# Performance work log

Measured on AMD Instinct MI355X. Metric: run time of the kernel, lower is better.

## Reference

```python
import jax, jax.numpy as jnp
import numpy as np

N_E, N_C, N_DL, N_IT, N_EP, N_HA, N_CA, N_AS = 11964, 188, 100, 7, 100, 10, 10, 7
D = 128
B, S = 256, 400
N_V = N_E + 1      # hypergraph vertices (exercises)
N_HE = N_C + 1     # hyperedges (concepts)
MEMB = 3           # concept memberships per exercise
BN_EPS = 1e-5


def _hg_v2v_mean(X, pair_v, pair_e):
    # HGNN+ smoothing: vertex -> hyperedge (mean) -> vertex (mean)
    ones_e = jnp.ones(pair_e.shape, X.dtype)
    e_deg = jnp.clip(jax.ops.segment_sum(ones_e, pair_e, num_segments=N_HE), 1.0)
    v_deg = jnp.clip(jax.ops.segment_sum(ones_e, pair_v, num_segments=N_V), 1.0)
    E = jax.ops.segment_sum(X[pair_v], pair_e, num_segments=N_HE) / e_deg[:, None]
    return jax.ops.segment_sum(E[pair_e], pair_v, num_segments=N_V) / v_deg[:, None]


def _hgnnp_conv(X, W, b, gamma, beta, mean, var, pair_v, pair_e, is_last):
    X = X @ W + b
    X = (X - mean) * jax.lax.rsqrt(var + BN_EPS) * gamma + beta  # eval-mode BN
    X = _hg_v2v_mean(X, pair_v, pair_e)
    if not is_last:
        X = jax.nn.relu(X)
    return X


def setup_inputs() -> dict:
    key = jax.random.key(0)
    ks = jax.random.split(key, 32)
    inp = {}
    inp['input_e'] = jax.random.randint(ks[0], (B, S), 0, N_V)
    inp['input_ed'] = jax.random.randint(ks[1], (B, S), 0, N_DL + 1)
    inp['input_ep'] = jax.random.randint(ks[2], (B, S), 0, N_EP + 1)
    inp['input_a'] = jax.random.randint(ks[3], (B, S), 0, 2)
    inp['input_as'] = jax.random.randint(ks[4], (B, S), 0, N_AS + 1)
    inp['input_ha'] = jax.random.randint(ks[5], (B, S), 0, N_HA + 1)
    inp['input_ca'] = jax.random.randint(ks[6], (B, S), 0, N_CA + 1)
    inp['input_it'] = jax.random.randint(ks[7], (B, S), 0, N_IT + 1)
    inp['deliver_h'] = jnp.zeros((B, D), jnp.float32)
    # hypergraph incidence (exercise-concept Q-matrix edges)
    rng = np.random.default_rng(0)
    inp['pair_v'] = jnp.asarray(np.repeat(np.arange(N_V), MEMB))
    inp['pair_e'] = jnp.asarray(rng.integers(0, N_HE, size=N_V * MEMB))
    inp['ec_map'] = jax.random.randint(ks[8], (N_V,), 0, N_HE)
    inp['ecd_map'] = jax.random.randint(ks[9], (N_V,), 0, N_DL + 1)
    # embedding tables (xavier-ish scale)
    def emb(k, n):
        return jax.random.normal(k, (n, D), jnp.float32) * 0.05
    inp['e_table'] = emb(ks[10], N_V)
    inp['c_table'] = emb(ks[11], N_HE)
    inp['ed_table'] = emb(ks[12], N_DL + 1)
    inp['cd_table'] = emb(ks[13], N_DL + 1)
    inp['a_table'] = emb(ks[14], 2)
    inp['it_table'] = emb(ks[15], N_IT + 1)
    inp['ep_table'] = emb(ks[16], N_EP + 1)
    inp['ha_table'] = emb(ks[17], N_HA + 1)
    inp['ca_table'] = emb(ks[18], N_CA + 1)
    inp['as_table'] = emb(ks[19], N_AS + 1)
    # HGNNP conv 1 & 2
    def lin(k, din, dout):
        return jax.random.normal(k, (din, dout), jnp.float32) * (1.0 / np.sqrt(din))
    inp['W1'] = lin(ks[20], D, D); inp['b1'] = jnp.zeros((D,), jnp.float32)
    inp['g1'] = jnp.ones((D,), jnp.float32); inp['be1'] = jnp.zeros((D,), jnp.float32)
    inp['m1'] = jnp.zeros((D,), jnp.float32); inp['v1'] = jnp.ones((D,), jnp.float32)
    inp['W2'] = lin(ks[21], D, D); inp['b2'] = jnp.zeros((D,), jnp.float32)
    inp['g2'] = jnp.ones((D,), jnp.float32); inp['be2'] = jnp.zeros((D,), jnp.float32)
    inp['m2'] = jnp.zeros((D,), jnp.float32); inp['v2'] = jnp.ones((D,), jnp.float32)
    # linear_i: (d_e + d_dl + d_ep + d_c + d_dl) -> d_x
    inp['Wi'] = lin(ks[22], 5 * D, D); inp['bi'] = jnp.zeros((D,), jnp.float32)
    # GRU knowledge-state cell: input = concat(x, a_emb) -> 2D, hidden D, 3 gates
    inp['Wg'] = lin(ks[23], 2 * D, 3 * D)
    inp['Ug'] = lin(ks[24], D, 3 * D)
    inp['bg'] = jnp.zeros((3 * D,), jnp.float32)
    # linear_predicting_e: d_x -> 1
    inp['We'] = lin(ks[25], D, 1); inp['beo'] = jnp.zeros((1,), jnp.float32)
    # linear_predicting_s: 4*d -> 1
    inp['Ws'] = lin(ks[26], 4 * D, 1); inp['bs'] = jnp.zeros((1,), jnp.float32)
    return inp


def reference(input_e, input_ed, input_ep, input_a, input_as, input_ha, input_ca, input_it,
              deliver_h, pair_v, pair_e, ec_map, ecd_map,
              e_table, c_table, ed_table, cd_table, a_table, it_table, ep_table,
              ha_table, ca_table, as_table,
              W1, b1, g1, be1, m1, v1, W2, b2, g2, be2, m2, v2,
              Wi, bi, Wg, Ug, bg, We, beo, Ws, bs):
    # 2-layer HGNN+ over the exercise hypergraph
    X = _hgnnp_conv(e_table, W1, b1, g1, be1, m1, v1, pair_v, pair_e, is_last=False)
    X = _hgnnp_conv(X, W2, b2, g2, be2, m2, v2, pair_v, pair_e, is_last=True)
    # embedding gathers  [B,S,D]
    e_emb = X[input_e]
    c_emb = c_table[ec_map[input_e]]
    cd_emb = cd_table[ecd_map[input_e]]
    ed_emb = ed_table[input_ed]
    ep_emb = ep_table[input_ep]
    x = jnp.tanh(jnp.concatenate([e_emb, ed_emb, ep_emb, c_emb, cd_emb], -1) @ Wi + bi)  # [B,S,D]
    a_emb = a_table[input_a]
    xs = jnp.moveaxis(jnp.concatenate([x, a_emb], -1), 1, 0)  # [S,B,2D]
    xp = jnp.moveaxis(x, 1, 0)                                # [S,B,D]

    def step(h, inputs):
        xin, xq = inputs
        y = jax.nn.sigmoid((h * xq) @ We + beo)[..., 0]  # predict from prior knowledge state
        gi = xin @ Wg + bg
        gh = h @ Ug
        iz, ir, inn = jnp.split(gi, 3, -1)
        hz, hr, hn = jnp.split(gh, 3, -1)
        z = jax.nn.sigmoid(iz + hz)
        r = jax.nn.sigmoid(ir + hr)
        n = jnp.tanh(inn + r * hn)
        return (1.0 - z) * n + z * h, y

    _, ys = jax.lax.scan(step, deliver_h, (xs, xp))
    pred_main = jnp.moveaxis(ys, 0, 1)  # [B,S]
    s_in = jnp.concatenate([ha_table[input_ha], ca_table[input_ca],
                            as_table[input_as], it_table[input_it]], -1)
    pred_s = jax.nn.sigmoid(s_in @ Ws + bs)[..., 0]  # [B,S]
    return pred_s, pred_main
```

## Files before the change

kernel.cpp:

```cpp
#include <hip/hip_runtime.h>

#define N_V   11965
#define N_HE  189
#define NPAIR 35895
#define BB    256
#define SS    400
#define DD    128
#define BSR   102400

typedef __bf16 bf16x8 __attribute__((ext_vector_type(8)));
typedef float  f32x4  __attribute__((ext_vector_type(4)));

__device__ __forceinline__ ushort f2bf(float f) {
    unsigned x = __float_as_uint(f);
    return (ushort)((x + 0x7FFFu + ((x >> 16) & 1u)) >> 16);
}
__device__ __forceinline__ float bf2f(ushort u) { return __uint_as_float(((unsigned)u) << 16); }
__device__ __forceinline__ float sigm(float x) { return 1.f / (1.f + __expf(-x)); }
__device__ __forceinline__ float tanh_f(float x) { return 2.f * sigm(2.f * x) - 1.f; }
__device__ __forceinline__ float blo(unsigned u) { return __uint_as_float(u << 16); }
__device__ __forceinline__ float bhi(unsigned u) { return __uint_as_float(u); }

struct P1Args {
    const int* pair_e;
    const float *b1, *g1, *be1, *m1, *v1;
    const float *b2, *g2, *be2, *m2, *v2;
    const float *W1, *W2, *Wi, *Wg, *Ug;
    const float *ed_t, *ep_t, *c_t, *cd_t, *a_t, *bi, *bg;
    const float *ha_t, *ca_t, *as_t, *it_t, *Ws;
    int* e_deg;
    float* aff;
    ushort *W1T, *W2T, *WiTe, *WgT, *UgT;
    float *edW, *epW, *cW, *cdW, *agi, *sd;
};

__global__ __launch_bounds__(384) void p1_kernel(P1Args A) {
    int bid = blockIdx.x, t = threadIdx.x;
    if (bid == 0) {
        if (t < 128) {
            float s = A.g1[t] * rsqrtf(A.v1[t] + 1e-5f);
            A.aff[t] = s;
            A.aff[128 + t] = A.b1[t] * s + A.be1[t] - A.m1[t] * s;
        } else if (t < 256) {
            int d = t - 128;
            float s = A.g2[d] * rsqrtf(A.v2[d] + 1e-5f);
            A.aff[256 + d] = s;
            A.aff[384 + d] = A.b2[d] * s + A.be2[d] - A.m2[d] * s;
        }
        return;
    }
    bid -= 1;
    if (bid < 94) {
        int p = bid * 384 + t;
        if (p < NPAIR) atomicAdd(&A.e_deg[A.pair_e[p]], 1);
        return;
    }
    bid -= 94;
    if (bid < 43) {
        int i = bid * 384 + t;
        if (i < 16384) { int k = i >> 7, n = i & 127; A.W1T[n * 128 + k] = f2bf(A.W1[i]); }
        return;
    }
    bid -= 43;
    if (bid < 43) {
        int i = bid * 384 + t;
        if (i < 16384) { int k = i >> 7, n = i & 127; A.W2T[n * 128 + k] = f2bf(A.W2[i]); }
        return;
    }
    bid -= 43;
    if (bid < 43) {
        int i = bid * 384 + t;
        if (i < 16384) { int k = i >> 7, n = i & 127; A.WiTe[n * 128 + k] = f2bf(A.Wi[i]); }
        return;
    }
    bid -= 43;
    if (bid < 128) {
        int i = bid * 384 + t;
        if (i < 49152) { int k = i / 384, n = i % 384; A.WgT[n * 128 + k] = f2bf(A.Wg[i]); }
        return;
    }
    bid -= 128;
    if (bid < 128) {
        int i = bid * 384 + t;
        if (i < 49152) { int k = i / 384, n = i % 384; A.UgT[n * 128 + k] = f2bf(A.Ug[i]); }
        return;
    }
    bid -= 128;
    if (bid < 101) {
        if (t < 128) {
            float acc = 0.f;
            for (int k = 0; k < 128; ++k)
                acc += A.ed_t[bid * 128 + k] * A.Wi[(128 + k) * 128 + t];
            A.edW[bid * 128 + t] = acc + A.bi[t];
        }
        return;
    }
    bid -= 101;
    if (bid < 101) {
        if (t < 128) {
            float acc = 0.f;
            for (int k = 0; k < 128; ++k)
                acc += A.ep_t[bid * 128 + k] * A.Wi[(256 + k) * 128 + t];
            A.epW[bid * 128 + t] = acc;
        }
        return;
    }
    bid -= 101;
    if (bid < 189) {
        if (t < 128) {
            float acc = 0.f;
            for (int k = 0; k < 128; ++k)
                acc += A.c_t[bid * 128 + k] * A.Wi[(384 + k) * 128 + t];
            A.cW[bid * 128 + t] = acc;
        }
        return;
    }
    bid -= 189;
    if (bid < 101) {
        if (t < 128) {
            float acc = 0.f;
            for (int k = 0; k < 128; ++k)
                acc += A.cd_t[bid * 128 + k] * A.Wi[(512 + k) * 128 + t];
            A.cdW[bid * 128 + t] = acc;
        }
        return;
    }
    bid -= 101;
    if (bid < 2) {
        float acc = 0.f;
        for (int k = 0; k < 128; ++k)
            acc += A.a_t[bid * 128 + k] * A.Wg[(128 + k) * 384 + t];
        A.agi[bid * 384 + t] = acc + A.bg[t];
        return;
    }
    bid -= 2;
    {
        int r = bid;
        const float* tab; int woff, row;
        if (r < 11)      { tab = A.ha_t; row = r;      woff = 0;   }
        else if (r < 22) { tab = A.ca_t; row = r - 11; woff = 128; }
        else if (r < 30) { tab = A.as_t; row = r - 22; woff = 256; }
        else             { tab = A.it_t; row = r - 30; woff = 384; }
        if (t < 64) {
            float p = tab[row * 128 + t] * A.Ws[woff + t]
                    + tab[row * 128 + 64 + t] * A.Ws[woff + 64 + t];
            #pragma unroll
            for (int o = 32; o > 0; o >>= 1) p += __shfl_xor(p, o);
            if (t == 0) A.sd[r] = p;
        }
    }
}

__global__ void cvt_kernel(const float* __restrict__ src, ushort* __restrict__ dst, int n) {
    int i = blockIdx.x * 256 + threadIdx.x;
    if (i < n) dst[i] = f2bf(src[i]);
}

__global__ void csr_prefix(const int* __restrict__ e_deg, int* __restrict__ start) {
    __shared__ int sc[256];
    int t = threadIdx.x;
    int d = (t < N_HE) ? e_deg[t] : 0;
    sc[t] = d;
    __syncthreads();
    for (int off = 1; off < 256; off <<= 1) {
        int v = (t >= off) ? sc[t - off] : 0;
        __syncthreads();
        sc[t] += v;
        __syncthreads();
    }
    if (t < N_HE) start[t] = sc[t] - d;
    if (t == N_HE - 1) start[N_HE] = sc[t];
}

__global__ void csr_fill(const int* __restrict__ pair_e, const int* __restrict__ pair_v,
                         const int* __restrict__ start, int* __restrict__ cursor,
                         int* __restrict__ list) {
    int p = blockIdx.x * 384 + threadIdx.x;
    if (p >= NPAIR) return;
    int e = pair_e[p];
    int pos = atomicAdd(&cursor[e], 1);
    list[start[e] + pos] = pair_v[p];
}

template <int NT>
__global__ __launch_bounds__(256) void gemm_mfma(
    const ushort* __restrict__ Amat, const ushort* __restrict__ BT,
    float* __restrict__ out, int M,
    const float* __restrict__ colS, const float* __restrict__ colB,
    const float* __restrict__ agi, const int* __restrict__ aidx) {
    const int N = NT * 16;
    int lane = threadIdx.x & 63, wave = threadIdx.x >> 6;
    int q = lane >> 4, c = lane & 15;
    int rowbase = blockIdx.x * 64 + wave * 16;
    int arow = rowbase + c;
    if (arow > M - 1) arow = M - 1;
    f32x4 acc[NT];
#pragma unroll
    for (int i = 0; i < NT; ++i) acc[i] = (f32x4){0.f, 0.f, 0.f, 0.f};
#pragma unroll
    for (int ko = 0; ko < 4; ++ko) {
        bf16x8 af = *(const bf16x8*)(Amat + (size_t)arow * 128 + ko * 32 + q * 8);
#pragma unroll
        for (int nt = 0; nt < NT; ++nt) {
            bf16x8 bfr = *(const bf16x8*)(BT + (size_t)(nt * 16 + c) * 128 + ko * 32 + q * 8);
            acc[nt] = __builtin_amdgcn_mfma_f32_16x16x32_bf16(af, bfr, acc[nt], 0, 0, 0);
        }
    }
#pragma unroll
    for (int nt = 0; nt < NT; ++nt) {
        int col = nt * 16 + c;
        float s = colS ? colS[col] : 1.f;
        float bb = colB ? colB[col] : 0.f;
#pragma unroll
        for (int r = 0; r < 4; ++r) {
            int row = rowbase + q * 4 + r;
            if (row < M) {
                float v = acc[nt][r] * s + bb;
                if (agi) v += agi[aidx[row] * N + col];
                out[(size_t)row * N + col] = v;
            }
        }
    }
}

__global__ __launch_bounds__(512) void edge_mean(const float* __restrict__ Y,
                                                 const int* __restrict__ list,
                                                 const int* __restrict__ start,
                                                 float* __restrict__ E) {
    __shared__ float red[4][128];
    int e = blockIdx.x;
    int d = threadIdx.x & 127, g = threadIdx.x >> 7;
    int s0 = start[e], n = start[e + 1] - s0;
    float acc = 0.f;
    for (int i = g; i < n; i += 4) acc += Y[(size_t)list[s0 + i] * DD + d];
    red[g][d] = acc;
    __syncthreads();
    if (g == 0) {
        float v = red[0][d] + red[1][d] + red[2][d] + red[3][d];
        E[e * DD + d] = v / (float)(n > 0 ? n : 1);
    }
}

__global__ void v_mean(const float* __restrict__ E, const int* __restrict__ pair_e,
                       ushort* __restrict__ Xo, int relu) {
    int idx = blockIdx.x * 256 + threadIdx.x;
    if (idx >= N_V * DD) return;
    int v = idx >> 7, d = idx & 127;
    float a = E[pair_e[3 * v] * DD + d] + E[pair_e[3 * v + 1] * DD + d] +
              E[pair_e[3 * v + 2] * DD + d];
    a *= (1.f / 3.f);
    if (relu) a = fmaxf(a, 0.f);
    Xo[idx] = f2bf(a);
}

__global__ void k3_kernel(const int* __restrict__ in_e, const int* __restrict__ in_ed,
                          const int* __restrict__ in_ep, const float* __restrict__ XW,
                          const float* __restrict__ cW, const float* __restrict__ cdW,
                          const float* __restrict__ edW, const float* __restrict__ epW,
                          const int* __restrict__ ec_map, const int* __restrict__ ecd_map,
                          ushort* __restrict__ xbf) {
    int idx = blockIdx.x * 256 + threadIdx.x;
    if (idx >= BSR * DD) return;
    int row = idx >> 7, d = idx & 127;
    int e = in_e[row];
    float v = XW[(size_t)e * DD + d] + cW[ec_map[e] * DD + d] + cdW[ecd_map[e] * DD + d] +
              edW[in_ed[row] * DD + d] + epW[in_ep[row] * DD + d];
    xbf[idx] = f2bf(tanh_f(v));
}

__global__ void pred_s_kernel(const int* __restrict__ ha, const int* __restrict__ ca,
                              const int* __restrict__ as_, const int* __restrict__ it,
                              const float* __restrict__ sd, const float* __restrict__ bs,
                              float* __restrict__ out) {
    int i = blockIdx.x * 256 + threadIdx.x;
    if (i >= BSR) return;
    float v = sd[ha[i]] + sd[11 + ca[i]] + sd[22 + as_[i]] + sd[30 + it[i]] + bs[0];
    out[i] = sigm(v);
}

__global__ void
__attribute__((amdgpu_flat_work_group_size(768, 768)))
gru_scan(
    const float* __restrict__ gi, const ushort* __restrict__ xb,
    const ushort* __restrict__ UgT, const float* __restrict__ h0,
    const float* __restrict__ We, const float* __restrict__ beo_p,
    float* __restrict__ out) {
    __shared__ __align__(16) float h_s[128];
    __shared__ float p_s[128];
    __shared__ float pp[4][392];
    int b = blockIdx.x, t = threadIdx.x;
    int kq = t / 192;
    int cp = t % 192;
    const uint4* WA = (const uint4*)(UgT + (size_t)cp * 128 + kq * 32);
    const uint4* WB = (const uint4*)(UgT + (size_t)(cp + 192) * 128 + kq * 32);
    uint4 A0 = WA[0], A1 = WA[1], A2 = WA[2], A3 = WA[3];
    uint4 B0 = WB[0], B1 = WB[1], B2 = WB[2], B3 = WB[3];
    unsigned a0 = A0.x, a1 = A0.y, a2 = A0.z, a3 = A0.w;
    unsigned a4 = A1.x, a5 = A1.y, a6 = A1.z, a7 = A1.w;
    unsigned a8 = A2.x, a9 = A2.y, a10 = A2.z, a11 = A2.w;
    unsigned a12 = A3.x, a13 = A3.y, a14 = A3.z, a15 = A3.w;
    unsigned c0 = B0.x, c1 = B0.y, c2 = B0.z, c3 = B0.w;
    unsigned c4 = B1.x, c5 = B1.y, c6 = B1.z, c7 = B1.w;
    unsigned c8 = B2.x, c9 = B2.y, c10 = B2.z, c11 = B2.w;
    unsigned c12 = B3.x, c13 = B3.y, c14 = B3.z, c15 = B3.w;
    float beo = beo_p[0];
    float wev = 0.f, hreg = 0.f;
    if (t < 128) {
        wev = We[t];
        hreg = h0[b * 128 + t];
        h_s[t] = hreg;
    }
    const float* gip = gi + (size_t)b * SS * 384;
    const ushort* xp = xb + (size_t)b * SS * 128;
    float gz_nx = 0.f, gr_nx = 0.f, gn_nx = 0.f, xw_nx = 0.f;
    if (t < 128) {
        gz_nx = gip[t];
        gr_nx = gip[128 + t];
        gn_nx = gip[256 + t];
        xw_nx = bf2f(xp[t]) * wev;
    }
    float* omain = out + BSR + b * SS;
    __syncthreads();
    for (int s = 0; s < SS; ++s) {
#define PINA(X) asm volatile("" : "+a"(X));
        PINA(a0) PINA(a1) PINA(a2) PINA(a3) PINA(a4) PINA(a5) PINA(a6) PINA(a7)
        PINA(a8) PINA(a9) PINA(a10) PINA(a11) PINA(a12) PINA(a13) PINA(a14) PINA(a15)
        PINA(c0) PINA(c1) PINA(c2) PINA(c3) PINA(c4) PINA(c5) PINA(c6) PINA(c7)
        PINA(c8) PINA(c9) PINA(c10) PINA(c11) PINA(c12) PINA(c13) PINA(c14) PINA(c15)
#undef PINA
        float gz = gz_nx, gr = gr_nx, gn = gn_nx, xw = xw_nx;
        if (s + 1 < SS && t < 128) {
            const float* g2 = gip + (size_t)(s + 1) * 384;
            gz_nx = g2[t];
            gr_nx = g2[128 + t];
            gn_nx = g2[256 + t];
            xw_nx = bf2f(xp[(size_t)(s + 1) * 128 + t]) * wev;
        }
        const float4* h4 = (const float4*)h_s + kq * 8;
        float accA = 0.f, accB = 0.f;
#define FB2(HI, U0, U1, U2, U3, V0, V1, V2, V3) { \
        float4 hv0 = h4[HI], hv1 = h4[HI + 1]; \
        accA = fmaf(hv0.x, blo(U0), accA); accA = fmaf(hv0.y, bhi(U0), accA); \
        accA = fmaf(hv0.z, blo(U1), accA); accA = fmaf(hv0.w, bhi(U1), accA); \
        accA = fmaf(hv1.x, blo(U2), accA); accA = fmaf(hv1.y, bhi(U2), accA); \
        accA = fmaf(hv1.z, blo(U3), accA); accA = fmaf(hv1.w, bhi(U3), accA); \
        accB = fmaf(hv0.x, blo(V0), accB); accB = fmaf(hv0.y, bhi(V0), accB); \
        accB = fmaf(hv0.z, blo(V1), accB); accB = fmaf(hv0.w, bhi(V1), accB); \
        accB = fmaf(hv1.x, blo(V2), accB); accB = fmaf(hv1.y, bhi(V2), accB); \
        accB = fmaf(hv1.z, blo(V3), accB); accB = fmaf(hv1.w, bhi(V3), accB); }
        FB2(0, a0, a1, a2, a3, c0, c1, c2, c3)
        FB2(2, a4, a5, a6, a7, c4, c5, c6, c7)
        FB2(4, a8, a9, a10, a11, c8, c9, c10, c11)
        FB2(6, a12, a13, a14, a15, c12, c13, c14, c15)
#undef FB2
        pp[kq][cp] = accA;
        pp[kq][cp + 192] = accB;
        if (t >= 704 && s > 0) {
            int l = t - 704;
            float pv = p_s[l] + p_s[l + 64];
#pragma unroll
            for (int o = 32; o > 0; o >>= 1) pv += __shfl_xor(pv, o);
            if (l == 0) omain[s - 1] = sigm(pv + beo);
        }
        __syncthreads();
        if (t < 128) {
            float Sz = pp[0][t] + pp[1][t] + pp[2][t] + pp[3][t];
            float Sr = pp[0][128 + t] + pp[1][128 + t] + pp[2][128 + t] + pp[3][128 + t];
            float Sn = pp[0][256 + t] + pp[1][256 + t] + pp[2][256 + t] + pp[3][256 + t];
            float z = sigm(gz + Sz);
            float r = sigm(gr + Sr);
            float n = tanh_f(gn + r * Sn);
            p_s[t] = hreg * xw;
            hreg = (1.f - z) * n + z * hreg;
            h_s[t] = hreg;
        }
        __syncthreads();
    }
    if (t >= 704) {
        int l = t - 704;
        float pv = p_s[l] + p_s[l + 64];
#pragma unroll
        for (int o = 32; o > 0; o >>= 1) pv += __shfl_xor(pv, o);
        if (l == 0) omain[SS - 1] = sigm(pv + beo);
    }
}

extern "C" void kernel_launch(void* const* d_in, const int* in_sizes, int n_in,
                              void* d_out, int out_size, void* d_ws, size_t ws_size,
                              hipStream_t stream) {
    const int* in_e   = (const int*)d_in[0];
    const int* in_ed  = (const int*)d_in[1];
    const int* in_ep  = (const int*)d_in[2];
    const int* in_a   = (const int*)d_in[3];
    const int* in_as  = (const int*)d_in[4];
    const int* in_ha  = (const int*)d_in[5];
    const int* in_ca  = (const int*)d_in[6];
    const int* in_it  = (const int*)d_in[7];
    const float* deliver_h = (const float*)d_in[8];
    const int* pair_v = (const int*)d_in[9];
    const int* pair_e = (const int*)d_in[10];
    const int* ec_map = (const int*)d_in[11];
    const int* ecd_map= (const int*)d_in[12];
    const float* e_table  = (const float*)d_in[13];
    const float* c_table  = (const float*)d_in[14];
    const float* ed_table = (const float*)d_in[15];
    const float* cd_table = (const float*)d_in[16];
    const float* a_table  = (const float*)d_in[17];
    const float* it_table = (const float*)d_in[18];
    const float* ep_table = (const float*)d_in[19];
    const float* ha_table = (const float*)d_in[20];
    const float* ca_table = (const float*)d_in[21];
    const float* as_table = (const float*)d_in[22];
    const float* W1 = (const float*)d_in[23];
    const float* b1 = (const float*)d_in[24];
    const float* g1 = (const float*)d_in[25];
    const float* be1= (const float*)d_in[26];
    const float* m1 = (const float*)d_in[27];
    const float* v1 = (const float*)d_in[28];
    const float* W2 = (const float*)d_in[29];
    const float* b2 = (const float*)d_in[30];
    const float* g2 = (const float*)d_in[31];
    const float* be2= (const float*)d_in[32];
    const float* m2 = (const float*)d_in[33];
    const float* v2 = (const float*)d_in[34];
    const float* Wi = (const float*)d_in[35];
    const float* bi = (const float*)d_in[36];
    const float* Wg = (const float*)d_in[37];
    const float* Ug = (const float*)d_in[38];
    const float* bg = (const float*)d_in[39];
    const float* We = (const float*)d_in[40];
    const float* beo= (const float*)d_in[41];
    const float* Ws = (const float*)d_in[42];
    const float* bs = (const float*)d_in[43];
    float* out = (float*)d_out;
    char* ws = (char*)d_ws;

    size_t off = 0;
    auto alloc = [&](size_t bytes) { size_t o = off; off += (bytes + 255) & ~(size_t)255; return o; };
    size_t o_degcur = alloc(378 * 4);
    size_t o_start  = alloc(190 * 4);
    size_t o_list   = alloc((size_t)NPAIR * 4);
    size_t o_aff    = alloc(512 * 4);
    size_t o_W1T    = alloc(16384 * 2);
    size_t o_W2T    = alloc(16384 * 2);
    size_t o_WiTe   = alloc(16384 * 2);
    size_t o_WgT    = alloc(49152 * 2);
    size_t o_UgT    = alloc(49152 * 2);
    size_t o_edW    = alloc(101 * 128 * 4);
    size_t o_epW    = alloc(101 * 128 * 4);
    size_t o_cW     = alloc(189 * 128 * 4);
    size_t o_cdW    = alloc(101 * 128 * 4);
    size_t o_agi    = alloc(2 * 384 * 4);
    size_t o_sd     = alloc(38 * 4);
    size_t o_etb    = alloc((size_t)N_V * DD * 2);
    size_t o_E      = alloc((size_t)N_HE * DD * 4);
    size_t o_Y      = alloc((size_t)N_V * DD * 4);
    size_t o_X1     = alloc((size_t)N_V * DD * 2);
    size_t o_X2     = alloc((size_t)N_V * DD * 2);
    size_t o_XW     = alloc((size_t)N_V * DD * 4);
    size_t o_xbf    = alloc((size_t)BSR * DD * 2);
    size_t o_gi     = alloc((size_t)BSR * 384 * 4);

    int*    e_deg  = (int*)(ws + o_degcur);
    int*    cursor = e_deg + 189;
    int*    startp = (int*)(ws + o_start);
    int*    listp  = (int*)(ws + o_list);
    float*  aff    = (float*)(ws + o_aff);
    ushort* W1T    = (ushort*)(ws + o_W1T);
    ushort* W2T    = (ushort*)(ws + o_W2T);
    ushort* WiTe   = (ushort*)(ws + o_WiTe);
    ushort* WgT    = (ushort*)(ws + o_WgT);
    ushort* UgTp   = (ushort*)(ws + o_UgT);
    float*  edW    = (float*)(ws + o_edW);
    float*  epW    = (float*)(ws + o_epW);
    float*  cW     = (float*)(ws + o_cW);
    float*  cdW    = (float*)(ws + o_cdW);
    float*  agi    = (float*)(ws + o_agi);
    float*  sd     = (float*)(ws + o_sd);
    ushort* e_tb   = (ushort*)(ws + o_etb);
    float*  E      = (float*)(ws + o_E);
    float*  Y      = (float*)(ws + o_Y);
    ushort* X1b    = (ushort*)(ws + o_X1);
    ushort* X2b    = (ushort*)(ws + o_X2);
    float*  XW     = (float*)(ws + o_XW);
    ushort* xbf    = (ushort*)(ws + o_xbf);
    float*  gi     = (float*)(ws + o_gi);

    hipMemsetAsync(ws + o_degcur, 0, 378 * 4, stream);

    P1Args pa;
    pa.pair_e = pair_e;
    pa.b1 = b1; pa.g1 = g1; pa.be1 = be1; pa.m1 = m1; pa.v1 = v1;
    pa.b2 = b2; pa.g2 = g2; pa.be2 = be2; pa.m2 = m2; pa.v2 = v2;
    pa.W1 = W1; pa.W2 = W2; pa.Wi = Wi; pa.Wg = Wg; pa.Ug = Ug;
    pa.ed_t = ed_table; pa.ep_t = ep_table; pa.c_t = c_table; pa.cd_t = cd_table;
    pa.a_t = a_table; pa.bi = bi; pa.bg = bg;
    pa.ha_t = ha_table; pa.ca_t = ca_table; pa.as_t = as_table; pa.it_t = it_table; pa.Ws = Ws;
    pa.e_deg = e_deg; pa.aff = aff;
    pa.W1T = W1T; pa.W2T = W2T; pa.WiTe = WiTe; pa.WgT = WgT; pa.UgT = UgTp;
    pa.edW = edW; pa.epW = epW; pa.cW = cW; pa.cdW = cdW; pa.agi = agi; pa.sd = sd;
    p1_kernel<<<1012, 384, 0, stream>>>(pa);

    cvt_kernel<<<(N_V * DD + 255) / 256, 256, 0, stream>>>(e_table, e_tb, N_V * DD);
    csr_prefix<<<1, 256, 0, stream>>>(e_deg, startp);
    csr_fill<<<94, 384, 0, stream>>>(pair_e, pair_v, startp, cursor, listp);

    pred_s_kernel<<<(BSR + 255) / 256, 256, 0, stream>>>(in_ha, in_ca, in_as, in_it, sd, bs, out);

    gemm_mfma<8><<<(N_V + 63) / 64, 256, 0, stream>>>(e_tb, W1T, Y, N_V, aff, aff + 128,
                                                      nullptr, nullptr);
    edge_mean<<<N_HE, 512, 0, stream>>>(Y, listp, startp, E);
    v_mean<<<(N_V * DD + 255) / 256, 256, 0, stream>>>(E, pair_e, X1b, 1);
    gemm_mfma<8><<<(N_V + 63) / 64, 256, 0, stream>>>(X1b, W2T, Y, N_V, aff + 256, aff + 384,
                                                      nullptr, nullptr);
    edge_mean<<<N_HE, 512, 0, stream>>>(Y, listp, startp, E);
    v_mean<<<(N_V * DD + 255) / 256, 256, 0, stream>>>(E, pair_e, X2b, 0);
    gemm_mfma<8><<<(N_V + 63) / 64, 256, 0, stream>>>(X2b, WiTe, XW, N_V, nullptr, nullptr,
                                                      nullptr, nullptr);
    k3_kernel<<<(BSR * DD + 255) / 256, 256, 0, stream>>>(in_e, in_ed, in_ep, XW, cW, cdW, edW,
                                                          epW, ec_map, ecd_map, xbf);
    gemm_mfma<24><<<BSR / 64, 256, 0, stream>>>(xbf, WgT, gi, BSR, nullptr, nullptr, agi, in_a);
    gru_scan<<<BB, 768, 0, stream>>>(gi, xbf, UgTp, deliver_h, We, beo, out);
}
```

Measured before the change: 976.5 us.

## Fuse setup kernels, store GRU input gates in bf16, vectorize gather kernel

Folds the e_table bf16 conversion into the setup kernel, merges the CSR prefix and fill into one kernel, and moves the pred_s computation into the gate GEMM epilogue, cutting the number of launches. The precomputed GRU input-gate tensor (BSR×384) is now written and read as bf16 instead of fp32, halving that large memory round trip. The embedding gather and tanh kernel now processes four columns per thread with float4 loads. Storing the gates in bf16 adds rounding error to the recurrent inputs.

```diff
diff --git a/kernel.cpp b/kernel.cpp
--- a/kernel.cpp
+++ b/kernel.cpp
@@ -7,6 +7,7 @@
 #define SS    400
 #define DD    128
 #define BSR   102400
+#define NVD   (N_V * DD)
 
 typedef __bf16 bf16x8 __attribute__((ext_vector_type(8)));
 typedef float  f32x4  __attribute__((ext_vector_type(4)));
@@ -25,12 +26,12 @@
     const int* pair_e;
     const float *b1, *g1, *be1, *m1, *v1;
     const float *b2, *g2, *be2, *m2, *v2;
-    const float *W1, *W2, *Wi, *Wg, *Ug;
+    const float *W1, *W2, *Wi, *Wg, *Ug, *e_t;
     const float *ed_t, *ep_t, *c_t, *cd_t, *a_t, *bi, *bg;
     const float *ha_t, *ca_t, *as_t, *it_t, *Ws;
     int* e_deg;
     float* aff;
-    ushort *W1T, *W2T, *WiTe, *WgT, *UgT;
+    ushort *W1T, *W2T, *WiTe, *WgT, *UgT, *e_tb;
     float *edW, *epW, *cW, *cdW, *agi, *sd;
 };
 
@@ -86,6 +87,17 @@
         return;
     }
     bid -= 128;
+    if (bid < 998) {
+        int i4 = bid * 1536 + t * 4;
+        if (i4 < NVD) {
+            float4 v = *(const float4*)(A.e_t + i4);
+            ushort4 o;
+            o.x = f2bf(v.x); o.y = f2bf(v.y); o.z = f2bf(v.z); o.w = f2bf(v.w);
+            *(ushort4*)(A.e_tb + i4) = o;
+        }
+        return;
+    }
+    bid -= 998;
     if (bid < 101) {
         if (t < 128) {
             float acc = 0.f;
@@ -151,75 +163,108 @@
     }
 }
 
-__global__ void cvt_kernel(const float* __restrict__ src, ushort* __restrict__ dst, int n) {
-    int i = blockIdx.x * 256 + threadIdx.x;
-    if (i < n) dst[i] = f2bf(src[i]);
-}
-
-__global__ void csr_prefix(const int* __restrict__ e_deg, int* __restrict__ start) {
+__global__ __launch_bounds__(384) void csr_build(
+    const int* __restrict__ e_deg, const int* __restrict__ pair_e,
+    const int* __restrict__ pair_v, int* __restrict__ start,
+    int* __restrict__ cursor, int* __restrict__ list) {
     __shared__ int sc[256];
+    __shared__ int sx[256];
     int t = threadIdx.x;
-    int d = (t < N_HE) ? e_deg[t] : 0;
-    sc[t] = d;
+    int d = 0;
+    if (t < 256) { d = (t < N_HE) ? e_deg[t] : 0; sc[t] = d; }
     __syncthreads();
     for (int off = 1; off < 256; off <<= 1) {
-        int v = (t >= off) ? sc[t - off] : 0;
+        int v = (t < 256 && t >= off) ? sc[t - off] : 0;
         __syncthreads();
-        sc[t] += v;
+        if (t < 256) sc[t] += v;
         __syncthreads();
     }
-    if (t < N_HE) start[t] = sc[t] - d;
-    if (t == N_HE - 1) start[N_HE] = sc[t];
-}
-
-__global__ void csr_fill(const int* __restrict__ pair_e, const int* __restrict__ pair_v,
-                         const int* __restrict__ start, int* __restrict__ cursor,
-                         int* __restrict__ list) {
-    int p = blockIdx.x * 384 + threadIdx.x;
-    if (p >= NPAIR) return;
-    int e = pair_e[p];
-    int pos = atomicAdd(&cursor[e], 1);
-    list[start[e] + pos] = pair_v[p];
-}
-
-template <int NT>
-__global__ __launch_bounds__(256) void gemm_mfma(
+    if (t < 256) sx[t] = sc[t] - d;
+    __syncthreads();
+    if (blockIdx.x == 0) {
+        if (t < N_HE) start[t] = sx[t];
+        if (t == 0) start[N_HE] = sc[N_HE - 1];
+    }
+    int p = blockIdx.x * 384 + t;
+    if (p < NPAIR) {
+        int e = pair_e[p];
+        int pos = atomicAdd(&cursor[e], 1);
+        list[sx[e] + pos] = pair_v[p];
+    }
+}
+
+__global__ __launch_bounds__(256) void gemm_mfma8(
     const ushort* __restrict__ Amat, const ushort* __restrict__ BT,
     float* __restrict__ out, int M,
-    const float* __restrict__ colS, const float* __restrict__ colB,
-    const float* __restrict__ agi, const int* __restrict__ aidx) {
-    const int N = NT * 16;
+    const float* __restrict__ colS, const float* __restrict__ colB) {
     int lane = threadIdx.x & 63, wave = threadIdx.x >> 6;
     int q = lane >> 4, c = lane & 15;
     int rowbase = blockIdx.x * 64 + wave * 16;
     int arow = rowbase + c;
     if (arow > M - 1) arow = M - 1;
-    f32x4 acc[NT];
-#pragma unroll
-    for (int i = 0; i < NT; ++i) acc[i] = (f32x4){0.f, 0.f, 0.f, 0.f};
+    f32x4 acc[8];
+#pragma unroll
+    for (int i = 0; i < 8; ++i) acc[i] = (f32x4){0.f, 0.f, 0.f, 0.f};
 #pragma unroll
     for (int ko = 0; ko < 4; ++ko) {
         bf16x8 af = *(const bf16x8*)(Amat + (size_t)arow * 128 + ko * 32 + q * 8);
 #pragma unroll
-        for (int nt = 0; nt < NT; ++nt) {
+        for (int nt = 0; nt < 8; ++nt) {
             bf16x8 bfr = *(const bf16x8*)(BT + (size_t)(nt * 16 + c) * 128 + ko * 32 + q * 8);
             acc[nt] = __builtin_amdgcn_mfma_f32_16x16x32_bf16(af, bfr, acc[nt], 0, 0, 0);
         }
     }
 #pragma unroll
-    for (int nt = 0; nt < NT; ++nt) {
+    for (int nt = 0; nt < 8; ++nt) {
         int col = nt * 16 + c;
         float s = colS ? colS[col] : 1.f;
         float bb = colB ? colB[col] : 0.f;
 #pragma unroll
         for (int r = 0; r < 4; ++r) {
             int row = rowbase + q * 4 + r;
-            if (row < M) {
-                float v = acc[nt][r] * s + bb;
-                if (agi) v += agi[aidx[row] * N + col];
-                out[(size_t)row * N + col] = v;
-            }
-        }
+            if (row < M) out[(size_t)row * 128 + col] = acc[nt][r] * s + bb;
+        }
+    }
+}
+
+__global__ __launch_bounds__(256) void gemm_gi(
+    const ushort* __restrict__ Amat, const ushort* __restrict__ BT,
+    ushort* __restrict__ out, const float* __restrict__ agi,
+    const int* __restrict__ aidx,
+    const int* __restrict__ ha, const int* __restrict__ ca,
+    const int* __restrict__ as_, const int* __restrict__ it,
+    const float* __restrict__ sd, const float* __restrict__ bs,
+    float* __restrict__ outs) {
+    int lane = threadIdx.x & 63, wave = threadIdx.x >> 6;
+    int q = lane >> 4, c = lane & 15;
+    int rowbase = blockIdx.x * 64 + wave * 16;
+    int arow = rowbase + c;
+    f32x4 acc[24];
+#pragma unroll
+    for (int i = 0; i < 24; ++i) acc[i] = (f32x4){0.f, 0.f, 0.f, 0.f};
+#pragma unroll
+    for (int ko = 0; ko < 4; ++ko) {
+        bf16x8 af = *(const bf16x8*)(Amat + (size_t)arow * 128 + ko * 32 + q * 8);
+#pragma unroll
+        for (int nt = 0; nt < 24; ++nt) {
+            bf16x8 bfr = *(const bf16x8*)(BT + (size_t)(nt * 16 + c) * 128 + ko * 32 + q * 8);
+            acc[nt] = __builtin_amdgcn_mfma_f32_16x16x32_bf16(af, bfr, acc[nt], 0, 0, 0);
+        }
+    }
+#pragma unroll
+    for (int nt = 0; nt < 24; ++nt) {
+        int col = nt * 16 + c;
+#pragma unroll
+        for (int r = 0; r < 4; ++r) {
+            int row = rowbase + q * 4 + r;
+            float v = acc[nt][r] + agi[aidx[row] * 384 + col];
+            out[(size_t)row * 384 + col] = f2bf(v);
+        }
+    }
+    if (threadIdx.x < 64) {
+        int row = blockIdx.x * 64 + threadIdx.x;
+        float v = sd[ha[row]] + sd[11 + ca[row]] + sd[22 + as_[row]] + sd[30 + it[row]] + bs[0];
+        outs[row] = sigm(v);
     }
 }
 
@@ -244,7 +289,7 @@
 __global__ void v_mean(const float* __restrict__ E, const int* __restrict__ pair_e,
                        ushort* __restrict__ Xo, int relu) {
     int idx = blockIdx.x * 256 + threadIdx.x;
-    if (idx >= N_V * DD) return;
+    if (idx >= NVD) return;
     int v = idx >> 7, d = idx & 127;
     float a = E[pair_e[3 * v] * DD + d] + E[pair_e[3 * v + 1] * DD + d] +
               E[pair_e[3 * v + 2] * DD + d];
@@ -260,28 +305,26 @@
                           const int* __restrict__ ec_map, const int* __restrict__ ecd_map,
                           ushort* __restrict__ xbf) {
     int idx = blockIdx.x * 256 + threadIdx.x;
-    if (idx >= BSR * DD) return;
-    int row = idx >> 7, d = idx & 127;
+    if (idx >= BSR * 32) return;
+    int row = idx >> 5, dq = (idx & 31) << 2;
     int e = in_e[row];
-    float v = XW[(size_t)e * DD + d] + cW[ec_map[e] * DD + d] + cdW[ecd_map[e] * DD + d] +
-              edW[in_ed[row] * DD + d] + epW[in_ep[row] * DD + d];
-    xbf[idx] = f2bf(tanh_f(v));
-}
-
-__global__ void pred_s_kernel(const int* __restrict__ ha, const int* __restrict__ ca,
-                              const int* __restrict__ as_, const int* __restrict__ it,
-                              const float* __restrict__ sd, const float* __restrict__ bs,
-                              float* __restrict__ out) {
-    int i = blockIdx.x * 256 + threadIdx.x;
-    if (i >= BSR) return;
-    float v = sd[ha[i]] + sd[11 + ca[i]] + sd[22 + as_[i]] + sd[30 + it[i]] + bs[0];
-    out[i] = sigm(v);
+    float4 a = *(const float4*)(XW + (size_t)e * DD + dq);
+    float4 b = *(const float4*)(cW + ec_map[e] * DD + dq);
+    float4 c = *(const float4*)(cdW + ecd_map[e] * DD + dq);
+    float4 d = *(const float4*)(edW + in_ed[row] * DD + dq);
+    float4 g = *(const float4*)(epW + in_ep[row] * DD + dq);
+    ushort4 o;
+    o.x = f2bf(tanh_f(a.x + b.x + c.x + d.x + g.x));
+    o.y = f2bf(tanh_f(a.y + b.y + c.y + d.y + g.y));
+    o.z = f2bf(tanh_f(a.z + b.z + c.z + d.z + g.z));
+    o.w = f2bf(tanh_f(a.w + b.w + c.w + d.w + g.w));
+    *(ushort4*)(xbf + (size_t)row * DD + dq) = o;
 }
 
 __global__ void
 __attribute__((amdgpu_flat_work_group_size(768, 768)))
 gru_scan(
-    const float* __restrict__ gi, const ushort* __restrict__ xb,
+    const ushort* __restrict__ gi, const ushort* __restrict__ xb,
     const ushort* __restrict__ UgT, const float* __restrict__ h0,
     const float* __restrict__ We, const float* __restrict__ beo_p,
     float* __restrict__ out) {
@@ -310,13 +353,13 @@
         hreg = h0[b * 128 + t];
         h_s[t] = hreg;
     }
-    const float* gip = gi + (size_t)b * SS * 384;
+    const ushort* gip = gi + (size_t)b * SS * 384;
     const ushort* xp = xb + (size_t)b * SS * 128;
     float gz_nx = 0.f, gr_nx = 0.f, gn_nx = 0.f, xw_nx = 0.f;
     if (t < 128) {
-        gz_nx = gip[t];
-        gr_nx = gip[128 + t];
-        gn_nx = gip[256 + t];
+        gz_nx = bf2f(gip[t]);
+        gr_nx = bf2f(gip[128 + t]);
+        gn_nx = bf2f(gip[256 + t]);
         xw_nx = bf2f(xp[t]) * wev;
     }
     float* omain = out + BSR + b * SS;
@@ -330,10 +373,10 @@
 #undef PINA
         float gz = gz_nx, gr = gr_nx, gn = gn_nx, xw = xw_nx;
         if (s + 1 < SS && t < 128) {
-            const float* g2 = gip + (size_t)(s + 1) * 384;
-            gz_nx = g2[t];
-            gr_nx = g2[128 + t];
-            gn_nx = g2[256 + t];
+            const ushort* g2 = gip + (size_t)(s + 1) * 384;
+            gz_nx = bf2f(g2[t]);
+            gr_nx = bf2f(g2[128 + t]);
+            gn_nx = bf2f(g2[256 + t]);
             xw_nx = bf2f(xp[(size_t)(s + 1) * 128 + t]) * wev;
         }
         const float4* h4 = (const float4*)h_s + kq * 8;
@@ -452,14 +495,14 @@
     size_t o_cdW    = alloc(101 * 128 * 4);
     size_t o_agi    = alloc(2 * 384 * 4);
     size_t o_sd     = alloc(38 * 4);
-    size_t o_etb    = alloc((size_t)N_V * DD * 2);
+    size_t o_etb    = alloc((size_t)NVD * 2);
     size_t o_E      = alloc((size_t)N_HE * DD * 4);
-    size_t o_Y      = alloc((size_t)N_V * DD * 4);
-    size_t o_X1     = alloc((size_t)N_V * DD * 2);
-    size_t o_X2     = alloc((size_t)N_V * DD * 2);
-    size_t o_XW     = alloc((size_t)N_V * DD * 4);
+    size_t o_Y      = alloc((size_t)NVD * 4);
+    size_t o_X1     = alloc((size_t)NVD * 2);
+    size_t o_X2     = alloc((size_t)NVD * 2);
+    size_t o_XW     = alloc((size_t)NVD * 4);
     size_t o_xbf    = alloc((size_t)BSR * DD * 2);
-    size_t o_gi     = alloc((size_t)BSR * 384 * 4);
+    size_t o_gi     = alloc((size_t)BSR * 384 * 2);
 
     int*    e_deg  = (int*)(ws + o_degcur);
     int*    cursor = e_deg + 189;
@@ -484,7 +527,7 @@
     ushort* X2b    = (ushort*)(ws + o_X2);
     float*  XW     = (float*)(ws + o_XW);
     ushort* xbf    = (ushort*)(ws + o_xbf);
-    float*  gi     = (float*)(ws + o_gi);
+    ushort* gi     = (ushort*)(ws + o_gi);
 
     hipMemsetAsync(ws + o_degcur, 0, 378 * 4, stream);
 
@@ -492,33 +535,27 @@
     pa.pair_e = pair_e;
     pa.b1 = b1; pa.g1 = g1; pa.be1 = be1; pa.m1 = m1; pa.v1 = v1;
     pa.b2 = b2; pa.g2 = g2; pa.be2 = be2; pa.m2 = m2; pa.v2 = v2;
-    pa.W1 = W1; pa.W2 = W2; pa.Wi = Wi; pa.Wg = Wg; pa.Ug = Ug;
+    pa.W1 = W1; pa.W2 = W2; pa.Wi = Wi; pa.Wg = Wg; pa.Ug = Ug; pa.e_t = e_table;
     pa.ed_t = ed_table; pa.ep_t = ep_table; pa.c_t = c_table; pa.cd_t = cd_table;
     pa.a_t = a_table; pa.bi = bi; pa.bg = bg;
     pa.ha_t = ha_table; pa.ca_t = ca_table; pa.as_t = as_table; pa.it_t = it_table; pa.Ws = Ws;
     pa.e_deg = e_deg; pa.aff = aff;
-    pa.W1T = W1T; pa.W2T = W2T; pa.WiTe = WiTe; pa.WgT = WgT; pa.UgT = UgTp;
+    pa.W1T = W1T; pa.W2T = W2T; pa.WiTe = WiTe; pa.WgT = WgT; pa.UgT = UgTp; pa.e_tb = e_tb;
     pa.edW = edW; pa.epW = epW; pa.cW = cW; pa.cdW = cdW; pa.agi = agi; pa.sd = sd;
-    p1_kernel<<<1012, 384, 0, stream>>>(pa);
-
-    cvt_kernel<<<(N_V * DD + 255) / 256, 256, 0, stream>>>(e_table, e_tb, N_V * DD);
-    csr_prefix<<<1, 256, 0, stream>>>(e_deg, startp);
-    csr_fill<<<94, 384, 0, stream>>>(pair_e, pair_v, startp, cursor, listp);
-
-    pred_s_kernel<<<(BSR + 255) / 256, 256, 0, stream>>>(in_ha, in_ca, in_as, in_it, sd, bs, out);
-
-    gemm_mfma<8><<<(N_V + 63) / 64, 256, 0, stream>>>(e_tb, W1T, Y, N_V, aff, aff + 128,
-                                                      nullptr, nullptr);
+    p1_kernel<<<2010, 384, 0, stream>>>(pa);
+
+    csr_build<<<94, 384, 0, stream>>>(e_deg, pair_e, pair_v, startp, cursor, listp);
+
+    gemm_mfma8<<<(N_V + 63) / 64, 256, 0, stream>>>(e_tb, W1T, Y, N_V, aff, aff + 128);
     edge_mean<<<N_HE, 512, 0, stream>>>(Y, listp, startp, E);
-    v_mean<<<(N_V * DD + 255) / 256, 256, 0, stream>>>(E, pair_e, X1b, 1);
-    gemm_mfma<8><<<(N_V + 63) / 64, 256, 0, stream>>>(X1b, W2T, Y, N_V, aff + 256, aff + 384,
-                                                      nullptr, nullptr);
+    v_mean<<<(NVD + 255) / 256, 256, 0, stream>>>(E, pair_e, X1b, 1);
+    gemm_mfma8<<<(N_V + 63) / 64, 256, 0, stream>>>(X1b, W2T, Y, N_V, aff + 256, aff + 384);
     edge_mean<<<N_HE, 512, 0, stream>>>(Y, listp, startp, E);
-    v_mean<<<(N_V * DD + 255) / 256, 256, 0, stream>>>(E, pair_e, X2b, 0);
-    gemm_mfma<8><<<(N_V + 63) / 64, 256, 0, stream>>>(X2b, WiTe, XW, N_V, nullptr, nullptr,
-                                                      nullptr, nullptr);
-    k3_kernel<<<(BSR * DD + 255) / 256, 256, 0, stream>>>(in_e, in_ed, in_ep, XW, cW, cdW, edW,
+    v_mean<<<(NVD + 255) / 256, 256, 0, stream>>>(E, pair_e, X2b, 0);
+    gemm_mfma8<<<(N_V + 63) / 64, 256, 0, stream>>>(X2b, WiTe, XW, N_V, nullptr, nullptr);
+    k3_kernel<<<(BSR * 32 + 255) / 256, 256, 0, stream>>>(in_e, in_ed, in_ep, XW, cW, cdW, edW,
                                                           epW, ec_map, ecd_map, xbf);
-    gemm_mfma<24><<<BSR / 64, 256, 0, stream>>>(xbf, WgT, gi, BSR, nullptr, nullptr, agi, in_a);
+    gemm_gi<<<BSR / 64, 256, 0, stream>>>(xbf, WgT, gi, agi, in_a,
+                                          in_ha, in_ca, in_as, in_it, sd, bs, out);
     gru_scan<<<BB, 768, 0, stream>>>(gi, xbf, UgTp, deliver_h, We, beo, out);
 }
```

New measurement: 912.1 us. 1.07x faster.
